# Kernel optimization log

Hardware: AMD Instinct MI355X
Metric: run time of the kernel (lower is better)

## Reference

```python
import jax, jax.numpy as jnp
import numpy as np
from jax import lax

# pywt Wavelet('db3') analysis filters (dec_lo, dec_hi)
DEC_LO = jnp.array([0.035226291882100656, -0.08544127388224149, -0.13501102001039084,
                    0.4598775021193313, 0.8068915093133388, 0.3326705529509569], dtype=jnp.float32)
DEC_HI = jnp.array([-0.3326705529509569, 0.8068915093133388, -0.4598775021193313,
                    -0.13501102001039084, 0.08544127388224149, 0.035226291882100656], dtype=jnp.float32)


def _dwt_level(x):
    # One analysis level of pytorch_wavelets DWT1D with mode='zero'.
    # x: [B, N] -> (lo, hi) each [B, (N+L-1)//2]
    N = x.shape[-1]
    L = DEC_LO.shape[0]
    outsize = (N + L - 1) // 2  # pywt.dwt_coeff_len, zero mode
    p = 2 * (outsize - 1) - N + L
    # conv_general_dilated does cross-correlation; reversed filter == true convolution
    w = jnp.stack([DEC_LO[::-1], DEC_HI[::-1]])[:, None, :]  # [2, 1, L]
    y = lax.conv_general_dilated(x[:, None, :], w, window_strides=(2,),
                                 padding=[(p // 2, p - p // 2)])  # [B, 2, outsize]
    return y[:, 0, :], y[:, 1, :]


def _wavelet_features(sig, level=3):
    # sig: [B, N]. Returns (mean of final low-pass, sum over levels of ||hf||_2) per row.
    lo = sig
    high = jnp.zeros(sig.shape[0], sig.dtype)
    for _ in range(level):
        lo, hi = _dwt_level(lo)
        high = high + jnp.sqrt(jnp.sum(hi * hi, axis=-1))
    return jnp.mean(lo, axis=-1), high


def _dirichlet_weight(low, high):
    # Deterministic surrogate: Dirichlet([a1*10, a2*10]) has mean a1/(a1+a2),
    # replacing scipy dirichlet.rvs sampling with its expectation.
    a1 = jnp.clip(low, 1e-6)
    a2 = jnp.clip(high, 1e-6)
    return a1 / (a1 + a2)


def _forward(user_idx, item_idx, values, num_users, num_items):
    # item popularity: scatter-add of values * log1p(interaction count), L2-normalized
    counts = jnp.zeros(num_items, jnp.float32).at[item_idx].add(1.0)
    log_counts = jnp.log1p(counts)
    pop = jnp.zeros(num_items, jnp.float32).at[item_idx].add(values * log_counts[item_idx])
    pop = pop / (jnp.linalg.norm(pop) + 1e-8)
    # user activity
    act = jnp.zeros(num_users, jnp.float32).at[user_idx].add(
        values / jnp.log1p(pop[item_idx] + 1e-8))
    act = act / (jnp.linalg.norm(act) + 1e-8)
    # dense per-entity interaction signals (batched scatter replaces per-entity masking loop)
    user_sig = jnp.zeros((num_users, num_items), jnp.float32).at[user_idx, item_idx].add(values)
    user_sig = user_sig * (1.0 + act)[:, None]
    item_sig = jnp.zeros((num_items, num_users), jnp.float32).at[item_idx, user_idx].add(values)
    item_sig = item_sig * (1.0 + pop)[:, None]
    u_low, u_high = _wavelet_features(user_sig)
    i_low, i_high = _wavelet_features(item_sig)
    u_pop = _dirichlet_weight(u_low, u_high)
    i_pop = _dirichlet_weight(i_low, i_high)
    u_ni, i_ni = 1.0 - u_pop, 1.0 - i_pop
    wu_p, wu_n = u_pop[user_idx], u_ni[user_idx]
    wi_p, wi_n = i_pop[item_idx], i_ni[item_idx]
    # nnz-valued sparse outputs: [UIPG(=pop/pop), UING(=niche/niche), pop/niche, niche/pop]
    return jnp.stack([values * wu_p * wi_p,
                      values * wu_n * wi_n,
                      values * wu_p * wi_n,
                      values * wu_n * wi_p])


def setup_inputs():
    key = jax.random.key(0)
    k1, k2, k3 = jax.random.split(key, 3)
    NNZ, U, I = 2_000_000, 8192, 8192
    return {
        "user_idx": jax.random.randint(k1, (NNZ,), 0, U, dtype=jnp.int32),
        "item_idx": jax.random.randint(k2, (NNZ,), 0, I, dtype=jnp.int32),
        "values": jax.random.uniform(k3, (NNZ,), dtype=jnp.float32),
        "num_users": U,
        "num_items": I,
    }


def reference(user_idx, item_idx, values, num_users, num_items):
    return _forward(user_idx, item_idx, values, num_users, num_items)
```

## Files before the change

kernel.cpp:

```cpp
#include <hip/hip_runtime.h>
#include <math.h>

#define NE 8192
#define HT 1024
#define NCH 8
#define RT 512
#define NROWS 16

__device__ __constant__ float LO_R[6] = {
    0.3326705529509569f, 0.8068915093133388f, 0.4598775021193313f,
    -0.13501102001039084f, -0.08544127388224149f, 0.035226291882100656f};
__device__ __constant__ float HI_RV[6] = {
    0.035226291882100656f, 0.08544127388224149f, -0.13501102001039084f,
    -0.4598775021193313f, 0.8068915093133388f, -0.3326705529509569f};

__device__ __forceinline__ float blockReduceSum(float v, float* red) {
    #pragma unroll
    for (int off = 32; off > 0; off >>= 1) v += __shfl_down(v, off);
    int lane = threadIdx.x & 63, wid = threadIdx.x >> 6;
    if (lane == 0) red[wid] = v;
    __syncthreads();
    float r = 0.f;
    if (threadIdx.x == 0) {
        int nw = blockDim.x >> 6;
        for (int i = 0; i < nw; ++i) r += red[i];
    }
    return r;
}

__global__ void k_tables(float* __restrict__ resp, float4* __restrict__ Tdiag) {
    int a = blockIdx.x * blockDim.x + threadIdx.x;
    if (a >= NE) return;
    float lo1r[8], hi1r[8];
    int k1a = max(0, (a >> 1) - 3);
    #pragma unroll
    for (int t = 0; t < 8; ++t) {
        int k = k1a + t;
        int j = a - 2 * k + 4;
        bool ok = (j >= 0 && j <= 5 && k <= 4097);
        lo1r[t] = ok ? LO_R[j] : 0.f;
        hi1r[t] = ok ? HI_RV[j] : 0.f;
    }
    float lo2r[8], hi2r[8];
    int k2a = max(0, (k1a >> 1) - 1);
    #pragma unroll
    for (int t = 0; t < 8; ++t) {
        int k = k2a + t;
        float aL = 0.f, aH = 0.f;
        if (k <= 2050) {
            #pragma unroll
            for (int j = 0; j < 6; ++j) {
                int idx = 2 * k - 4 + j - k1a;
                if (idx >= 0 && idx < 8) {
                    aL = fmaf(LO_R[j], lo1r[idx], aL);
                    aH = fmaf(HI_RV[j], lo1r[idx], aH);
                }
            }
        }
        lo2r[t] = aL; hi2r[t] = aH;
    }
    float lo3r[8], hi3r[8];
    int k3a = max(0, (k2a >> 1) - 1);
    #pragma unroll
    for (int t = 0; t < 8; ++t) {
        int k = k3a + t;
        float aL = 0.f, aH = 0.f;
        if (k <= 1027) {
            #pragma unroll
            for (int j = 0; j < 6; ++j) {
                int idx = 2 * k - 4 + j - k2a;
                if (idx >= 0 && idx < 8) {
                    aL = fmaf(LO_R[j], lo2r[idx], aL);
                    aH = fmaf(HI_RV[j], lo2r[idx], aH);
                }
            }
        }
        lo3r[t] = aL; hi3r[t] = aH;
    }
    float g1 = 0.f, g2 = 0.f, g3 = 0.f, w3 = 0.f;
    #pragma unroll
    for (int t = 0; t < 8; ++t) {
        g1 = fmaf(hi1r[t], hi1r[t], g1);
        g2 = fmaf(hi2r[t], hi2r[t], g2);
        g3 = fmaf(hi3r[t], hi3r[t], g3);
        w3 += lo3r[t];
    }
    Tdiag[a] = make_float4(w3, g1, g2, g3);
    float* rp = resp + (size_t)a * 32;
    #pragma unroll
    for (int t = 0; t < 8; ++t) { rp[t] = hi1r[t]; rp[8 + t] = hi2r[t]; rp[16 + t] = hi3r[t]; }
    rp[24] = __int_as_float(k1a);
    rp[25] = __int_as_float(k2a);
    rp[26] = __int_as_float(k3a);
}

__global__ void k_gram(const float* __restrict__ resp, float* __restrict__ Gt) {
    int idx = blockIdx.x * 256 + threadIdx.x;
    if (idx >= NE * 35) return;
    int a = idx / 35;
    int d = idx - a * 35 + 1;
    int b = a + d;
    float v1 = 0.f, v2 = 0.f, v3 = 0.f;
    const float* ra = resp + (size_t)a * 32;
    if (b < NE) {
        const float* rb = resp + (size_t)b * 32;
        {
            int s = __float_as_int(rb[26]) - __float_as_int(ra[26]);
            #pragma unroll
            for (int u = 0; u < 8; ++u) {
                int t = u + s;
                if (t >= 0 && t < 8) v3 = fmaf(rb[16 + u], ra[16 + t], v3);
            }
        }
        if (d <= 15) {
            int s = __float_as_int(rb[25]) - __float_as_int(ra[25]);
            #pragma unroll
            for (int u = 0; u < 8; ++u) {
                int t = u + s;
                if (t >= 0 && t < 8) v2 = fmaf(rb[8 + u], ra[8 + t], v2);
            }
        }
        if (d <= 5) {
            int s = __float_as_int(rb[24]) - __float_as_int(ra[24]);
            #pragma unroll
            for (int u = 0; u < 8; ++u) {
                int t = u + s;
                if (t >= 0 && t < 8) v1 = fmaf(rb[u], ra[t], v1);
            }
        }
    }
    float* g = Gt + (size_t)a * 56;
    if (d <= 5)  g[d - 1] = v1;
    if (d <= 15) g[5 + d - 1] = v2;
    g[20 + d - 1] = v3;
}

__global__ __launch_bounds__(HT) void k_hist3(const int* __restrict__ ui,
                                              const int* __restrict__ ii,
                                              const float* __restrict__ v, int nnz,
                                              int* __restrict__ sliceU,
                                              int* __restrict__ sliceI,
                                              float* __restrict__ sliceS) {
    __shared__ int hU[NE];
    __shared__ int hI[NE];
    __shared__ float hS[NE];
    int b = blockIdx.x, tid = threadIdx.x, hb = gridDim.x;
    int4* hU4 = (int4*)hU; int4* hI4 = (int4*)hI; int4* hS4 = (int4*)hS;
    int4 z4 = make_int4(0, 0, 0, 0);
    for (int j = tid; j < NE / 4; j += HT) { hU4[j] = z4; hI4[j] = z4; hS4[j] = z4; }
    __syncthreads();
    int C = (nnz + hb - 1) / hb;
    int beg = b * C, end = min(nnz, beg + C);
    for (int n = beg + tid; n < end; n += HT) {
        atomicAdd(&hU[ui[n]], 1);
        int it = ii[n];
        atomicAdd(&hI[it], 1);
        atomicAdd(&hS[it], v[n]);
    }
    __syncthreads();
    size_t base = (size_t)b * NE;
    int4* sU = (int4*)(sliceU + base); int4* sI = (int4*)(sliceI + base);
    int4* sS = (int4*)(sliceS + base);
    for (int j = tid; j < NE / 4; j += HT) { sU[j] = hU4[j]; sI[j] = hI4[j]; sS[j] = hS4[j]; }
}

__global__ void k_chunksum3(const int* __restrict__ sliceU, const int* __restrict__ sliceI,
                            const float* __restrict__ sliceS, int spc,
                            int* __restrict__ csU, int* __restrict__ csI,
                            float* __restrict__ csS) {
    int i = blockIdx.x * 256 + threadIdx.x;
    int c = blockIdx.y;
    int b0 = c * spc;
    int cu = 0, ci = 0; float sv = 0.f;
    for (int b = b0; b < b0 + spc; ++b) {
        size_t o = (size_t)b * NE + i;
        cu += sliceU[o]; ci += sliceI[o]; sv += sliceS[o];
    }
    size_t oc = (size_t)c * NE + i;
    csU[oc] = cu; csI[oc] = ci; csS[oc] = sv;
}

__global__ void k_final3(const int* __restrict__ csU, const int* __restrict__ csI,
                         const float* __restrict__ csS,
                         int* cntU, int* cntI, float* popraw, float* normAcc) {
    __shared__ float red[4];
    int i = blockIdx.x * 256 + threadIdx.x;
    int cu = 0, ci = 0; float sv = 0.f;
    #pragma unroll
    for (int c = 0; c < NCH; ++c) {
        size_t o = (size_t)c * NE + i;
        cu += csU[o]; ci += csI[o]; sv += csS[o];
    }
    cntU[i] = cu; cntI[i] = ci;
    float p = log1pf((float)ci) * sv;
    popraw[i] = p;
    float s = blockReduceSum(p * p, red);
    if (threadIdx.x == 0) atomicAdd(&normAcc[0], s);
}

__global__ void k_scan2(const int* __restrict__ cntU, const int* __restrict__ cntI,
                        int* ptrU, int* ptrI) {
    __shared__ int sums[256];
    const int* cnt = blockIdx.x ? cntI : cntU;
    int* ptr = blockIdx.x ? ptrI : ptrU;
    int tid = threadIdx.x;
    int base = tid * 32;
    int local[32];
    int s = 0;
    #pragma unroll
    for (int j = 0; j < 32; ++j) { local[j] = cnt[base + j]; s += local[j]; }
    sums[tid] = s;
    __syncthreads();
    for (int off = 1; off < 256; off <<= 1) {
        int t = (tid >= off) ? sums[tid - off] : 0;
        __syncthreads();
        sums[tid] += t;
        __syncthreads();
    }
    int run = (tid > 0) ? sums[tid - 1] : 0;
    #pragma unroll
    for (int j = 0; j < 32; ++j) { ptr[base + j] = run; run += local[j]; }
    if (tid == 255) ptr[NE] = run;
}

__global__ void k_colscanB(int* csU, int* csI,
                           const int* __restrict__ ptrU, const int* __restrict__ ptrI) {
    int i = blockIdx.x * 256 + threadIdx.x;
    int* cs = blockIdx.y ? csI : csU;
    const int* ptr = blockIdx.y ? ptrI : ptrU;
    int run = ptr[i];
    #pragma unroll
    for (int c = 0; c < NCH; ++c) {
        size_t o = (size_t)c * NE + i;
        int t = cs[o]; cs[o] = run; run += t;
    }
}

__global__ void k_colscanC(int* sliceU, int* sliceI,
                           const int* __restrict__ csU, const int* __restrict__ csI, int spc) {
    int i = blockIdx.x * 256 + threadIdx.x;
    int c = blockIdx.y;
    int* slice = blockIdx.z ? sliceI : sliceU;
    const int* cs = blockIdx.z ? csI : csU;
    int run = cs[(size_t)c * NE + i];
    int b0 = c * spc;
    for (int b = b0; b < b0 + spc; ++b) {
        size_t o = (size_t)b * NE + i;
        int t = slice[o]; slice[o] = run; run += t;
    }
}

__global__ __launch_bounds__(HT) void k_scatter2(const int* __restrict__ ui,
                                                 const int* __restrict__ ii,
                                                 const float* __restrict__ v, int nnz,
                                                 const int* __restrict__ sliceU,
                                                 const int* __restrict__ sliceI,
                                                 const float* __restrict__ popraw,
                                                 const float* __restrict__ normAcc,
                                                 int2* __restrict__ pairsU,
                                                 int2* __restrict__ pairsI,
                                                 float* __restrict__ sliceA) {
    __shared__ int curU[NE];
    __shared__ int curI[NE];
    __shared__ float hA[NE];
    int b = blockIdx.x, tid = threadIdx.x, hb = gridDim.x;
    const int4* sU = (const int4*)(sliceU + (size_t)b * NE);
    const int4* sI = (const int4*)(sliceI + (size_t)b * NE);
    int4* cU4 = (int4*)curU; int4* cI4 = (int4*)curI;
    float4* hA4 = (float4*)hA;
    float4 zf = make_float4(0.f, 0.f, 0.f, 0.f);
    for (int j = tid; j < NE / 4; j += HT) { cU4[j] = sU[j]; cI4[j] = sI[j]; hA4[j] = zf; }
    __syncthreads();
    float rs0 = 1.f / (sqrtf(normAcc[0]) + 1e-8f);
    int C = (nnz + hb - 1) / hb;
    int beg = b * C, end = min(nnz, beg + C);
    for (int n = beg + tid; n < end; n += HT) {
        int u = ui[n], it = ii[n];
        float val = v[n];
        atomicAdd(&hA[u], val / log1pf(popraw[it] * rs0 + 1e-8f));
        int pU = atomicAdd(&curU[u], 1);
        pairsU[pU] = make_int2(it, __float_as_int(val));
        int pI = atomicAdd(&curI[it], 1);
        pairsI[pI] = make_int2(u, __float_as_int(val));
    }
    __syncthreads();
    float4* sA = (float4*)(sliceA + (size_t)b * NE);
    for (int j = tid; j < NE / 4; j += HT) sA[j] = hA4[j];
}

__global__ void k_actchunk(const float* __restrict__ sliceA, int spc, float* __restrict__ csA) {
    int i = blockIdx.x * 256 + threadIdx.x;
    int c = blockIdx.y;
    int b0 = c * spc;
    float a = 0.f;
    for (int b = b0; b < b0 + spc; ++b) a += sliceA[(size_t)b * NE + i];
    csA[(size_t)c * NE + i] = a;
}

__global__ void k_actfinal(const float* __restrict__ csA, float* act, float* normAcc) {
    __shared__ float red[4];
    int i = blockIdx.x * 256 + threadIdx.x;
    float a = 0.f;
    #pragma unroll
    for (int c = 0; c < NCH; ++c) a += csA[(size_t)c * NE + i];
    act[i] = a;
    float s = blockReduceSum(a * a, red);
    if (threadIdx.x == 0) atomicAdd(&normAcc[1], s);
}

__device__ __forceinline__ void scan_one(int p, float v, float4 td,
                                         const float* __restrict__ X,
                                         const unsigned int* __restrict__ M,
                                         const float* __restrict__ Gt,
                                         float& s1, float& s2, float& s3, float& ls) {
    float xp = X[p];
    ls = fmaf(v, td.x, ls);
    float vx = v * xp;
    s1 = fmaf(vx, td.y, s1);
    s2 = fmaf(vx, td.z, s2);
    s3 = fmaf(vx, td.w, s3);
    int w = p >> 5, sh = (p & 31) + 1;
    unsigned long long lo64 = (unsigned long long)M[w] |
                              ((unsigned long long)M[w + 1] << 32);
    unsigned long long win = (lo64 >> sh) |
                             ((unsigned long long)M[w + 2] << (64 - sh));
    win &= (1ull << 35) - 1ull;
    const float* g = Gt + (size_t)p * 56;
    while (win) {
        int d = __ffsll((unsigned long long)win);
        win &= win - 1;
        float c = 2.f * v * X[p + d];
        s3 = fmaf(c, g[19 + d], s3);
        if (d <= 15) s2 = fmaf(c, g[4 + d], s2);
        if (d <= 5)  s1 = fmaf(c, g[d - 1], s1);
    }
}

__global__ __launch_bounds__(RT) void k_rows(const int* __restrict__ ptrU,
                                             const int* __restrict__ ptrI,
                                             const int2* __restrict__ pairsU,
                                             const int2* __restrict__ pairsI,
                                             const float* __restrict__ popraw,
                                             const float* __restrict__ actraw,
                                             const float* __restrict__ normAcc,
                                             const float4* __restrict__ Tdiag,
                                             const float* __restrict__ Gt,
                                             float* __restrict__ u_w,
                                             float* __restrict__ i_w) {
    __shared__ __align__(16) float X[NE];
    __shared__ unsigned int M[260];
    __shared__ float acc[NROWS][4];
    int tid = threadIdx.x;
    int bid = blockIdx.x;
    bool isUser = bid >= 512;
    int r0 = (isUser ? bid - 512 : bid) * NROWS;
    const int* ptr = isUser ? ptrU : ptrI;
    const int2* pairs = isUser ? pairsU : pairsI;
    const float* raw = isUser ? actraw : popraw;
    float* w_out = isUser ? u_w : i_w;
    float rs = 1.f / (sqrtf(normAcc[isUser ? 1 : 0]) + 1e-8f);

    float4* X4 = (float4*)X;
    const float4 z4 = make_float4(0.f, 0.f, 0.f, 0.f);
    for (int q = tid; q < NE / 4; q += RT) X4[q] = z4;
    if (tid < 260) M[tid] = 0u;
    if (tid < NROWS * 4) ((float*)acc)[tid] = 0.f;

    int beg = ptr[r0], end = ptr[r0 + 1];
    int2 pr = make_int2(0, 0);
    float4 td = z4;
    if (tid < end - beg) {
        pr = pairs[beg + tid];
        td = Tdiag[pr.x];
    }

    for (int j = 0; j < NROWS; ++j) {
        int rl = r0 + j;
        __syncthreads();

        int cnt = end - beg;
        if (tid < cnt) {
            int p = pr.x;
            atomicAdd(&X[p], __int_as_float(pr.y));
            atomicOr(&M[p >> 5], 1u << (p & 31));
        }
        for (int n = beg + RT + tid; n < end; n += RT) {
            int2 q2 = pairs[n];
            atomicAdd(&X[q2.x], __int_as_float(q2.y));
            atomicOr(&M[q2.x >> 5], 1u << (q2.x & 31));
        }
        __syncthreads();

        int begN = end, endN = end;
        int2 prN = make_int2(0, 0);
        float4 tdN = z4;
        if (j + 1 < NROWS) {
            endN = ptr[rl + 2];
            if (tid < endN - begN) {
                prN = pairs[begN + tid];
                tdN = Tdiag[prN.x];
            }
        }

        float s1 = 0.f, s2 = 0.f, s3 = 0.f, ls = 0.f;
        if (tid < cnt)
            scan_one(pr.x, __int_as_float(pr.y), td, X, M, Gt, s1, s2, s3, ls);
        for (int n = beg + RT + tid; n < end; n += RT) {
            int2 q2 = pairs[n];
            scan_one(q2.x, __int_as_float(q2.y), Tdiag[q2.x], X, M, Gt, s1, s2, s3, ls);
        }

        #pragma unroll
        for (int off = 32; off > 0; off >>= 1) {
            s1 += __shfl_down(s1, off);
            s2 += __shfl_down(s2, off);
            s3 += __shfl_down(s3, off);
            ls += __shfl_down(ls, off);
        }
        if ((tid & 63) == 0) {
            atomicAdd(&acc[j][0], s1);
            atomicAdd(&acc[j][1], s2);
            atomicAdd(&acc[j][2], s3);
            atomicAdd(&acc[j][3], ls);
        }
        __syncthreads();

        if (tid < cnt) { X[pr.x] = 0.f; M[pr.x >> 5] = 0u; }
        for (int n = beg + RT + tid; n < end; n += RT) {
            int2 q2 = pairs[n];
            X[q2.x] = 0.f; M[q2.x >> 5] = 0u;
        }
        beg = begN; end = endN; pr = prN; td = tdN;
    }

    __syncthreads();
    if (tid < NROWS) {
        float t1 = acc[tid][0], t2 = acc[tid][1], t3 = acc[tid][2], tl = acc[tid][3];
        float rawv = raw[r0 + tid];
        float sc = 1.f + rawv * rs;
        float high = (sqrtf(fmaxf(t1, 0.f)) + sqrtf(fmaxf(t2, 0.f)) +
                      sqrtf(fmaxf(t3, 0.f))) * sc;
        float low = tl * (1.f / 1028.f) * sc;
        float a1 = fmaxf(low, 1e-6f);
        float a2 = fmaxf(high, 1e-6f);
        w_out[r0 + tid] = a1 / (a1 + a2);
    }
}

__global__ void k_out(const int* __restrict__ ui, const int* __restrict__ ii,
                      const float* __restrict__ v, int nnz,
                      const float* __restrict__ u_w, const float* __restrict__ i_w,
                      float* __restrict__ out) {
    int ngroups = nnz >> 2;
    int idx = blockIdx.x * blockDim.x + threadIdx.x;
    int stride = gridDim.x * blockDim.x;
    const int4* ui4 = (const int4*)ui;
    const int4* ii4 = (const int4*)ii;
    const float4* v4 = (const float4*)v;
    float4* o0 = (float4*)out;
    float4* o1 = (float4*)(out + (size_t)nnz);
    float4* o2 = (float4*)(out + 2 * (size_t)nnz);
    float4* o3 = (float4*)(out + 3 * (size_t)nnz);
    for (int g = idx; g < ngroups; g += stride) {
        int4 u = ui4[g];
        int4 it = ii4[g];
        float4 val = v4[g];
        float wu0 = u_w[u.x], wu1 = u_w[u.y], wu2 = u_w[u.z], wu3 = u_w[u.w];
        float wi0 = i_w[it.x], wi1 = i_w[it.y], wi2 = i_w[it.z], wi3 = i_w[it.w];
        o0[g] = make_float4(val.x * wu0 * wi0, val.y * wu1 * wi1,
                            val.z * wu2 * wi2, val.w * wu3 * wi3);
        o1[g] = make_float4(val.x * (1.f - wu0) * (1.f - wi0), val.y * (1.f - wu1) * (1.f - wi1),
                            val.z * (1.f - wu2) * (1.f - wi2), val.w * (1.f - wu3) * (1.f - wi3));
        o2[g] = make_float4(val.x * wu0 * (1.f - wi0), val.y * wu1 * (1.f - wi1),
                            val.z * wu2 * (1.f - wi2), val.w * wu3 * (1.f - wi3));
        o3[g] = make_float4(val.x * (1.f - wu0) * wi0, val.y * (1.f - wu1) * wi1,
                            val.z * (1.f - wu2) * wi2, val.w * (1.f - wu3) * wi3);
    }
    int tail = ngroups * 4;
    for (int n = tail + idx; n < nnz; n += stride) {
        float val = v[n];
        float wu = u_w[ui[n]], wi = i_w[ii[n]];
        out[n] = val * wu * wi;
        out[(size_t)nnz + n] = val * (1.f - wu) * (1.f - wi);
        out[2 * (size_t)nnz + n] = val * wu * (1.f - wi);
        out[3 * (size_t)nnz + n] = val * (1.f - wu) * wi;
    }
}

extern "C" void kernel_launch(void* const* d_in, const int* in_sizes, int n_in,
                              void* d_out, int out_size, void* d_ws, size_t ws_size,
                              hipStream_t stream) {
    const int* ui = (const int*)d_in[0];
    const int* ii = (const int*)d_in[1];
    const float* vals = (const float*)d_in[2];
    int nnz = in_sizes[0];
    float* out = (float*)d_out;

    char* ws = (char*)d_ws;
    size_t off = 0;
    auto take = [&](size_t bytes) -> char* {
        char* p = ws + off;
        off = (off + bytes + 255) & ~(size_t)255;
        return p;
    };

    int*   cntU    = (int*)take(NE * 4);
    int*   cntI    = (int*)take(NE * 4);
    float* popraw  = (float*)take(NE * 4);
    float* actraw  = (float*)take(NE * 4);
    int*   ptrU    = (int*)take((NE + 1) * 4);
    int*   ptrI    = (int*)take((NE + 1) * 4);
    float* u_w     = (float*)take(NE * 4);
    float* i_w     = (float*)take(NE * 4);
    float* normAcc = (float*)take(256);
    float4* Tdiag  = (float4*)take((size_t)NE * 16);
    float* Gt      = (float*)take((size_t)NE * 56 * 4);
    float* resp    = (float*)take((size_t)NE * 32 * 4);
    int*   csU     = (int*)take((size_t)NCH * NE * 4);
    int*   csI     = (int*)take((size_t)NCH * NE * 4);
    float* csS     = (float*)take((size_t)NCH * NE * 4);
    int2*  pairsU  = (int2*)take((size_t)nnz * 8);
    int2*  pairsI  = (int2*)take((size_t)nnz * 8);
    size_t fixedEnd = off;

    int hb = 256;
    while (hb > 8 && fixedEnd + 3 * (size_t)hb * NE * 4 + 4096 > ws_size) hb >>= 1;
    int spc = hb / NCH;
    int*   sliceU = (int*)take((size_t)hb * NE * 4);
    int*   sliceI = (int*)take((size_t)hb * NE * 4);
    float* sliceS = (float*)take((size_t)hb * NE * 4);

    hipMemsetAsync(normAcc, 0, 256, stream);

    int nb = (nnz / 4 + 255) / 256;
    if (nb > 2048) nb = 2048;

    k_tables<<<NE / 64, 64, 0, stream>>>(resp, Tdiag);
    k_gram<<<(NE * 35 + 255) / 256, 256, 0, stream>>>(resp, Gt);

    k_hist3<<<hb, HT, 0, stream>>>(ui, ii, vals, nnz, sliceU, sliceI, sliceS);
    k_chunksum3<<<dim3(32, NCH), 256, 0, stream>>>(sliceU, sliceI, sliceS, spc, csU, csI, csS);
    k_final3<<<32, 256, 0, stream>>>(csU, csI, csS, cntU, cntI, popraw, normAcc);

    k_scan2<<<2, 256, 0, stream>>>(cntU, cntI, ptrU, ptrI);
    k_colscanB<<<dim3(32, 2), 256, 0, stream>>>(csU, csI, ptrU, ptrI);
    k_colscanC<<<dim3(32, NCH, 2), 256, 0, stream>>>(sliceU, sliceI, csU, csI, spc);

    k_scatter2<<<hb, HT, 0, stream>>>(ui, ii, vals, nnz, sliceU, sliceI,
                                      popraw, normAcc, pairsU, pairsI, sliceS);

    k_actchunk<<<dim3(32, NCH), 256, 0, stream>>>(sliceS, spc, csS);
    k_actfinal<<<32, 256, 0, stream>>>(csS, actraw, normAcc);

    k_rows<<<1024, RT, 0, stream>>>(ptrU, ptrI, pairsU, pairsI,
                                    popraw, actraw, normAcc, Tdiag, Gt, u_w, i_w);

    k_out<<<nb, 256, 0, stream>>>(ui, ii, vals, nnz, u_w, i_w, out);
}
```

Baseline: 239.5 us.

## Double-buffer row bitmask and pack Gram table as float4 to drop a barrier

The Gram table is now stored as one float4 per diagonal offset (v1, v2, v3), so the scan loop does a single vector load instead of three scalar loads with branches. In the row kernel the occupancy bitmask is double-buffered. The previous row's entries are removed by atomic subtraction and bit clearing in the same phase as inserting the next row, which removes one __syncthreads per row. The tradeoffs are a larger Gram table (35 float4 per entry instead of 56 floats), extra atomics in place of plain stores, and X being restored by subtraction, which may not return exactly to zero in float.

```diff
diff --git a/kernel.cpp b/kernel.cpp
--- a/kernel.cpp
+++ b/kernel.cpp
@@ -94,7 +94,7 @@
     rp[26] = __int_as_float(k3a);
 }
 
-__global__ void k_gram(const float* __restrict__ resp, float* __restrict__ Gt) {
+__global__ void k_gram(const float* __restrict__ resp, float4* __restrict__ Gt4) {
     int idx = blockIdx.x * 256 + threadIdx.x;
     if (idx >= NE * 35) return;
     int a = idx / 35;
@@ -129,10 +129,7 @@
             }
         }
     }
-    float* g = Gt + (size_t)a * 56;
-    if (d <= 5)  g[d - 1] = v1;
-    if (d <= 15) g[5 + d - 1] = v2;
-    g[20 + d - 1] = v3;
+    Gt4[(size_t)a * 35 + d - 1] = make_float4(v1, v2, v3, 0.f);
 }
 
 __global__ __launch_bounds__(HT) void k_hist3(const int* __restrict__ ui,
@@ -310,8 +307,8 @@
 
 __device__ __forceinline__ void scan_one(int p, float v, float4 td,
                                          const float* __restrict__ X,
-                                         const unsigned int* __restrict__ M,
-                                         const float* __restrict__ Gt,
+                                         const unsigned int* __restrict__ Mrow,
+                                         const float4* __restrict__ Gt4,
                                          float& s1, float& s2, float& s3, float& ls) {
     float xp = X[p];
     ls = fmaf(v, td.x, ls);
@@ -320,19 +317,20 @@
     s2 = fmaf(vx, td.z, s2);
     s3 = fmaf(vx, td.w, s3);
     int w = p >> 5, sh = (p & 31) + 1;
-    unsigned long long lo64 = (unsigned long long)M[w] |
-                              ((unsigned long long)M[w + 1] << 32);
+    unsigned long long lo64 = (unsigned long long)Mrow[w] |
+                              ((unsigned long long)Mrow[w + 1] << 32);
     unsigned long long win = (lo64 >> sh) |
-                             ((unsigned long long)M[w + 2] << (64 - sh));
+                             ((unsigned long long)Mrow[w + 2] << (64 - sh));
     win &= (1ull << 35) - 1ull;
-    const float* g = Gt + (size_t)p * 56;
+    const float4* g = Gt4 + (size_t)p * 35 - 1;
     while (win) {
         int d = __ffsll((unsigned long long)win);
         win &= win - 1;
         float c = 2.f * v * X[p + d];
-        s3 = fmaf(c, g[19 + d], s3);
-        if (d <= 15) s2 = fmaf(c, g[4 + d], s2);
-        if (d <= 5)  s1 = fmaf(c, g[d - 1], s1);
+        float4 G = g[d];
+        s1 = fmaf(c, G.x, s1);
+        s2 = fmaf(c, G.y, s2);
+        s3 = fmaf(c, G.z, s3);
     }
 }
 
@@ -344,11 +342,11 @@
                                              const float* __restrict__ actraw,
                                              const float* __restrict__ normAcc,
                                              const float4* __restrict__ Tdiag,
-                                             const float* __restrict__ Gt,
+                                             const float4* __restrict__ Gt4,
                                              float* __restrict__ u_w,
                                              float* __restrict__ i_w) {
     __shared__ __align__(16) float X[NE];
-    __shared__ unsigned int M[260];
+    __shared__ unsigned int M[2][264];
     __shared__ float acc[NROWS][4];
     int tid = threadIdx.x;
     int bid = blockIdx.x;
@@ -363,7 +361,7 @@
     float4* X4 = (float4*)X;
     const float4 z4 = make_float4(0.f, 0.f, 0.f, 0.f);
     for (int q = tid; q < NE / 4; q += RT) X4[q] = z4;
-    if (tid < 260) M[tid] = 0u;
+    if (tid < 264) { M[0][tid] = 0u; M[1][tid] = 0u; }
     if (tid < NROWS * 4) ((float*)acc)[tid] = 0.f;
 
     int beg = ptr[r0], end = ptr[r0 + 1];
@@ -373,23 +371,38 @@
         pr = pairs[beg + tid];
         td = Tdiag[pr.x];
     }
+    int begPrev = 0, endPrev = 0;
+    int2 prPrev = make_int2(0, 0);
 
     for (int j = 0; j < NROWS; ++j) {
         int rl = r0 + j;
-        __syncthreads();
-
+        unsigned int* Mrow = M[j & 1];
+        unsigned int* Mold = M[(j ^ 1) & 1];
+
+        if (j > 0) {
+            int cntP = endPrev - begPrev;
+            if (tid < cntP) {
+                int p = prPrev.x;
+                atomicAdd(&X[p], -__int_as_float(prPrev.y));
+                atomicAnd(&Mold[p >> 5], ~(1u << (p & 31)));
+            }
+            for (int n = begPrev + RT + tid; n < endPrev; n += RT) {
+                int2 q2 = pairs[n];
+                atomicAdd(&X[q2.x], -__int_as_float(q2.y));
+                atomicAnd(&Mold[q2.x >> 5], ~(1u << (q2.x & 31)));
+            }
+        }
         int cnt = end - beg;
         if (tid < cnt) {
             int p = pr.x;
             atomicAdd(&X[p], __int_as_float(pr.y));
-            atomicOr(&M[p >> 5], 1u << (p & 31));
+            atomicOr(&Mrow[p >> 5], 1u << (p & 31));
         }
         for (int n = beg + RT + tid; n < end; n += RT) {
             int2 q2 = pairs[n];
             atomicAdd(&X[q2.x], __int_as_float(q2.y));
-            atomicOr(&M[q2.x >> 5], 1u << (q2.x & 31));
-        }
-        __syncthreads();
+            atomicOr(&Mrow[q2.x >> 5], 1u << (q2.x & 31));
+        }
 
         int begN = end, endN = end;
         int2 prN = make_int2(0, 0);
@@ -401,13 +414,15 @@
                 tdN = Tdiag[prN.x];
             }
         }
+        __syncthreads();
 
         float s1 = 0.f, s2 = 0.f, s3 = 0.f, ls = 0.f;
         if (tid < cnt)
-            scan_one(pr.x, __int_as_float(pr.y), td, X, M, Gt, s1, s2, s3, ls);
+            scan_one(pr.x, __int_as_float(pr.y), td, X, Mrow, Gt4, s1, s2, s3, ls);
         for (int n = beg + RT + tid; n < end; n += RT) {
             int2 q2 = pairs[n];
-            scan_one(q2.x, __int_as_float(q2.y), Tdiag[q2.x], X, M, Gt, s1, s2, s3, ls);
+            scan_one(q2.x, __int_as_float(q2.y), Tdiag[q2.x], X, Mrow, Gt4,
+                     s1, s2, s3, ls);
         }
 
         #pragma unroll
@@ -425,15 +440,10 @@
         }
         __syncthreads();
 
-        if (tid < cnt) { X[pr.x] = 0.f; M[pr.x >> 5] = 0u; }
-        for (int n = beg + RT + tid; n < end; n += RT) {
-            int2 q2 = pairs[n];
-            X[q2.x] = 0.f; M[q2.x >> 5] = 0u;
-        }
+        begPrev = beg; endPrev = end; prPrev = pr;
         beg = begN; end = endN; pr = prN; td = tdN;
     }
 
-    __syncthreads();
     if (tid < NROWS) {
         float t1 = acc[tid][0], t2 = acc[tid][1], t3 = acc[tid][2], tl = acc[tid][3];
         float rawv = raw[r0 + tid];
@@ -514,7 +524,7 @@
     float* i_w     = (float*)take(NE * 4);
     float* normAcc = (float*)take(256);
     float4* Tdiag  = (float4*)take((size_t)NE * 16);
-    float* Gt      = (float*)take((size_t)NE * 56 * 4);
+    float4* Gt4    = (float4*)take((size_t)NE * 35 * 16);
     float* resp    = (float*)take((size_t)NE * 32 * 4);
     int*   csU     = (int*)take((size_t)NCH * NE * 4);
     int*   csI     = (int*)take((size_t)NCH * NE * 4);
@@ -536,7 +546,7 @@
     if (nb > 2048) nb = 2048;
 
     k_tables<<<NE / 64, 64, 0, stream>>>(resp, Tdiag);
-    k_gram<<<(NE * 35 + 255) / 256, 256, 0, stream>>>(resp, Gt);
+    k_gram<<<(NE * 35 + 255) / 256, 256, 0, stream>>>(resp, Gt4);
 
     k_hist3<<<hb, HT, 0, stream>>>(ui, ii, vals, nnz, sliceU, sliceI, sliceS);
     k_chunksum3<<<dim3(32, NCH), 256, 0, stream>>>(sliceU, sliceI, sliceS, spc, csU, csI, csS);
@@ -553,7 +563,7 @@
     k_actfinal<<<32, 256, 0, stream>>>(csS, actraw, normAcc);
 
     k_rows<<<1024, RT, 0, stream>>>(ptrU, ptrI, pairsU, pairsI,
-                                    popraw, actraw, normAcc, Tdiag, Gt, u_w, i_w);
+                                    popraw, actraw, normAcc, Tdiag, Gt4, u_w, i_w);
 
     k_out<<<nb, 256, 0, stream>>>(ui, ii, vals, nnz, u_w, i_w, out);
 }
```

Result: slower. 261.4 us (+9.1%).
